# Kernel tuning notes

Hardware: AMD Instinct MI355X
Metric: run time of the kernel (lower is better)

The kernel has to match this reference:

```python
import jax, jax.numpy as jnp
import numpy as np

BLOCK = 16          # NVFP4 block size along contraction dim
FP4_MAX = 6.0       # max magnitude of E2M1
FP8_MAX = 448.0     # max magnitude of float8_e4m3fn

_LEVELS = jnp.array([0.0, 0.5, 1.0, 1.5, 2.0, 3.0, 4.0, 6.0], dtype=jnp.float32)
_MIDS   = jnp.array([0.25, 0.75, 1.25, 1.75, 2.5, 3.5, 5.0], dtype=jnp.float32)


def quantize_dequant_nvfp4(t, global_scale):
    """Fake-quantize t (last dim % 16 == 0) to NVFP4: per-16-block fp8-e4m3
    scale times global fp32 scale, values snapped to the E2M1 grid."""
    shp = t.shape
    tb = t.reshape(shp[:-1] + (shp[-1] // BLOCK, BLOCK))
    amax = jnp.max(jnp.abs(tb), axis=-1, keepdims=True)
    # per-block scale, quantized to float8_e4m3fn as in TensorCoreNVFP4Layout
    bs = amax / (FP4_MAX * global_scale)
    bs8 = bs.astype(jnp.float8_e4m3fn).astype(jnp.float32)
    scale = bs8 * global_scale                       # effective dequant scale
    v = tb / jnp.maximum(scale, 1e-12)
    sign = jnp.sign(v)
    a = jnp.clip(jnp.abs(v), 0.0, FP4_MAX)
    idx = jnp.sum(a[..., None] > _MIDS, axis=-1)     # nearest E2M1 level
    q = _LEVELS[idx] * sign * scale
    return q.reshape(shp)


def setup_inputs() -> dict:
    key = jax.random.key(0)
    kx, kw, kb = jax.random.split(key, 3)
    x = jax.random.normal(kx, (8192, 4096), dtype=jnp.float32)
    weight = jax.random.normal(kw, (4096, 4096), dtype=jnp.float32) * 0.02
    bias = jax.random.normal(kb, (4096,), dtype=jnp.float32) * 0.02
    # global scales (weight_scale_2 / input_scale): amax / (6 * 448)
    input_scale = jnp.max(jnp.abs(x)) / (FP4_MAX * FP8_MAX)
    weight_scale = jnp.max(jnp.abs(weight)) / (FP4_MAX * FP8_MAX)
    return {"x": x, "weight": weight, "bias": bias,
            "input_scale": input_scale, "weight_scale": weight_scale}


def reference(x, weight, bias, input_scale, weight_scale):
    xq = quantize_dequant_nvfp4(x, input_scale)      # [T, K]
    wq = quantize_dequant_nvfp4(weight, weight_scale)  # [N, K]
    return jnp.einsum('tk,nk->tn', xq, wq) + bias    # F.linear
```

## Files before the change

### kernel.cpp

```cpp
#include <hip/hip_runtime.h>
#include <hip/hip_bf16.h>
#include <stdint.h>

typedef __attribute__((ext_vector_type(8))) __bf16 bf16x8;
typedef __attribute__((ext_vector_type(4))) float f32x4;

#define BM 256
#define BN 256
#define BKT 32
#define SLOT 16384


__device__ __forceinline__ float fp8_e4m3_rne(float x) {
  if (x < 0.015625f) {
    return rintf(x * 512.0f) * 0.001953125f;
  }
  uint32_t u = __float_as_uint(x);
  uint32_t keep = u & 0xFFF00000u;
  uint32_t rem  = u & 0x000FFFFFu;
  uint32_t lsb  = (u >> 20) & 1u;
  if (rem > 0x80000u || (rem == 0x80000u && lsb)) keep += 0x100000u;
  return __uint_as_float(keep);
}

__device__ __forceinline__ float snap_lvl(float a) {
  if (a > 5.0f)  return 6.0f;
  if (a > 3.5f)  return 4.0f;
  if (a > 2.5f)  return 3.0f;
  if (a > 1.75f) return 2.0f;
  if (a > 1.25f) return 1.5f;
  if (a > 0.75f) return 1.0f;
  if (a > 0.25f) return 0.5f;
  return 0.0f;
}

__global__ __launch_bounds__(256) void quant_nvfp4(
    const float* __restrict__ in, unsigned short* __restrict__ out,
    const float* __restrict__ gsp, int nblk) {
  int b = blockIdx.x * 256 + threadIdx.x;
  if (b >= nblk) return;
  float gs = gsp[0];
  const float4* p = reinterpret_cast<const float4*>(in) + (size_t)b * 4;
  float v[16];
#pragma unroll
  for (int i = 0; i < 4; ++i) {
    float4 t4 = p[i];
    v[i * 4 + 0] = t4.x; v[i * 4 + 1] = t4.y;
    v[i * 4 + 2] = t4.z; v[i * 4 + 3] = t4.w;
  }
  float amax = 0.0f;
#pragma unroll
  for (int i = 0; i < 16; ++i) amax = fmaxf(amax, fabsf(v[i]));
  float bs8 = fp8_e4m3_rne(amax / (6.0f * gs));
  float scale = fmaxf(bs8 * gs, 1e-12f);
  unsigned short o[16];
#pragma unroll
  for (int i = 0; i < 16; ++i) {
    float q = v[i] / scale;
    float a = fminf(fabsf(q), 6.0f);
    float val = copysignf(snap_lvl(a) * bs8, q);
    o[i] = (unsigned short)(__float_as_uint(val) >> 16);
  }
  uint4 w0 = make_uint4((uint32_t)o[0] | ((uint32_t)o[1] << 16),
                        (uint32_t)o[2] | ((uint32_t)o[3] << 16),
                        (uint32_t)o[4] | ((uint32_t)o[5] << 16),
                        (uint32_t)o[6] | ((uint32_t)o[7] << 16));
  uint4 w1 = make_uint4((uint32_t)o[8]  | ((uint32_t)o[9]  << 16),
                        (uint32_t)o[10] | ((uint32_t)o[11] << 16),
                        (uint32_t)o[12] | ((uint32_t)o[13] << 16),
                        (uint32_t)o[14] | ((uint32_t)o[15] << 16));
  uint4* op = reinterpret_cast<uint4*>(out + (size_t)b * 16);
  op[0] = w0;
  op[1] = w1;
}


__device__ __forceinline__ void async_lds16(const void* g, void* l) {
  __builtin_amdgcn_global_load_lds((__attribute__((address_space(1))) void*)(g),
                                   (__attribute__((address_space(3))) void*)(l),
                                   16, 0, 0);
}

#define SB asm volatile("" ::: "memory")
#define VMC(S) asm volatile("s_waitcnt vmcnt(" S ")" ::: "memory")

#define STAGE_TILE(s, so) {                                                    \
    char* _la = (char*)As + (so);                                              \
    char* _lb = (char*)Bs + (so);                                              \
    async_lds16(pA0 + (size_t)(s) * BKT, _la + lo0);                           \
    async_lds16(pB0 + (size_t)(s) * BKT, _lb + lo0);                           \
    async_lds16(pA1 + (size_t)(s) * BKT, _la + lo1);                           \
    async_lds16(pB1 + (size_t)(s) * BKT, _lb + lo1);                           \
  }

#define CTILE(SOFF) do {                                                       \
    bf16x8 bfr[4], afr[8];                                                     \
    _Pragma("unroll") for (int ni = 0; ni < 4; ++ni)                           \
      bfr[ni] = *(const bf16x8*)((const char*)Bs + offB[ni] + (SOFF));         \
    _Pragma("unroll") for (int mi = 0; mi < 8; ++mi)                           \
      afr[mi] = *(const bf16x8*)((const char*)As + offA[mi] + (SOFF));         \
    _Pragma("unroll") for (int mi = 0; mi < 8; ++mi)                           \
      _Pragma("unroll") for (int ni = 0; ni < 4; ++ni)                         \
        acc[mi][ni] = __builtin_amdgcn_mfma_f32_16x16x32_bf16(                 \
            afr[mi], bfr[ni], acc[mi][ni], 0, 0, 0);                           \
  } while (0)

__global__ __launch_bounds__(512, 2) void gemm_bt_bf16(
    const unsigned short* __restrict__ A, const unsigned short* __restrict__ B,
    const float* __restrict__ bias, const float* __restrict__ gsx,
    const float* __restrict__ gsw, float* __restrict__ C,
    int M, int N, int K) {
  __shared__ __align__(16) unsigned short As[5 * 8192];
  __shared__ __align__(16) unsigned short Bs[5 * 8192];

  const int t = threadIdx.x;
  const int l = t & 63;
  const int w = t >> 6;
  const int wm = w >> 2, wn = w & 3;

  const int nbn = N / BN;
  const int nwg = (M / BM) * nbn;
  const int cpx = nwg >> 3;
  int bid = blockIdx.x;
  int logical = (bid & 7) * cpx + (bid >> 3);
  const int bm = logical / nbn, bn = logical % nbn;
  const int brow = bm * BM, bcol = bn * BN;

  unsigned int b0 = (unsigned int)t * 16u;
  unsigned int b1 = b0 + 8192u;
  unsigned int bp0 = b0 ^ (((b0 >> 7) & 3u) << 4);
  unsigned int bp1 = b1 ^ (((b1 >> 7) & 3u) << 4);
  const unsigned int lo0 = b0, lo1 = b1;
  const unsigned short* pA0 = A + (size_t)(brow + (bp0 >> 6)) * K + ((bp0 & 63u) >> 1);
  const unsigned short* pA1 = A + (size_t)(brow + (bp1 >> 6)) * K + ((bp1 & 63u) >> 1);
  const unsigned short* pB0 = B + (size_t)(bcol + (bp0 >> 6)) * K + ((bp0 & 63u) >> 1);
  const unsigned short* pB1 = B + (size_t)(bcol + (bp1 >> 6)) * K + ((bp1 & 63u) >> 1);

  unsigned int offA[8], offB[4];
#pragma unroll
  for (int mi = 0; mi < 8; ++mi) {
    unsigned int r = wm * 128 + mi * 16 + (l & 15);
    unsigned int q = r * 64 + ((l >> 4) << 4);
    offA[mi] = q ^ (((q >> 7) & 3u) << 4);
  }
#pragma unroll
  for (int ni = 0; ni < 4; ++ni) {
    unsigned int r = wn * 64 + ni * 16 + (l & 15);
    unsigned int q = r * 64 + ((l >> 4) << 4);
    offB[ni] = q ^ (((q >> 7) & 3u) << 4);
  }

  f32x4 acc[8][4] = {};

  STAGE_TILE(0, 0);
  STAGE_TILE(1, SLOT);
  STAGE_TILE(2, 2 * SLOT);

  int sa = 0;
#pragma unroll 1
  for (int w2 = 0; w2 < 62; ++w2) {
    int T = 2 * w2;
    int sb = sa + 1; if (sb >= 5) sb -= 5;
    int s3 = sa + 3; if (s3 >= 5) s3 -= 5;
    int s4 = sa + 4; if (s4 >= 5) s4 -= 5;
    SB; VMC("4"); __builtin_amdgcn_s_barrier(); SB;
    STAGE_TILE(T + 3, s3 * SLOT);
    CTILE(sa * SLOT);
    STAGE_TILE(T + 4, s4 * SLOT);
    CTILE(sb * SLOT);
    sa += 2; if (sa >= 5) sa -= 5;
  }
  SB; VMC("4"); __builtin_amdgcn_s_barrier(); SB;
  STAGE_TILE(127, 2 * SLOT);
  CTILE(4 * SLOT);
  CTILE(0 * SLOT);
  SB; VMC("0"); __builtin_amdgcn_s_barrier(); SB;
  CTILE(1 * SLOT);
  CTILE(2 * SLOT);

  const float gscale = gsx[0] * gsw[0];
  float bias_r[4];
#pragma unroll
  for (int ni = 0; ni < 4; ++ni)
    bias_r[ni] = bias[bcol + wn * 64 + ni * 16 + (l & 15)];
#pragma unroll
  for (int mi = 0; mi < 8; ++mi) {
#pragma unroll
    for (int ni = 0; ni < 4; ++ni) {
#pragma unroll
      for (int r = 0; r < 4; ++r) {
        int row = brow + wm * 128 + mi * 16 + (l >> 4) * 4 + r;
        int col = bcol + wn * 64 + ni * 16 + (l & 15);
        C[(size_t)row * N + col] = acc[mi][ni][r] * gscale + bias_r[ni];
      }
    }
  }
}


extern "C" void kernel_launch(void* const* d_in, const int* in_sizes, int n_in,
                              void* d_out, int out_size, void* d_ws, size_t ws_size,
                              hipStream_t stream) {
  const float* x    = (const float*)d_in[0];
  const float* wgt  = (const float*)d_in[1];
  const float* bias = (const float*)d_in[2];
  const float* isc  = (const float*)d_in[3];
  const float* wsc  = (const float*)d_in[4];
  float* out = (float*)d_out;

  const int N = in_sizes[2];
  const int K = in_sizes[1] / N;
  const int M = in_sizes[0] / K;

  unsigned short* Aq = (unsigned short*)d_ws;
  unsigned short* Bq = Aq + (size_t)M * K;

  int nblkA = M * K / 16;
  quant_nvfp4<<<(nblkA + 255) / 256, 256, 0, stream>>>(x, Aq, isc, nblkA);
  int nblkB = N * K / 16;
  quant_nvfp4<<<(nblkB + 255) / 256, 256, 0, stream>>>(wgt, Bq, wsc, nblkB);

  dim3 grid((M / BM) * (N / BN));
  gemm_bt_bf16<<<grid, 512, 0, stream>>>(Aq, Bq, bias, isc, wsc, out, M, N, K);
}
```

Measured before the change: 337.2 us.

## Pack quantized weights in MFMA fragment order and load B directly to registers

The weight quantizer now writes B in a pre-packed layout that matches the MFMA fragment order. This lets the GEMM load B fragments straight from global memory into registers with double-buffered register sets, skipping the LDS staging for B. The A operand keeps LDS staging but moves to a 3-slot ring, and uses inline ds_read with fine-grained lgkmcnt waits, sched barriers and setprio so MFMAs can interleave with LDS reads. This frees LDS and cuts LDS traffic, but B global loads are now issued per wave, so latency hiding depends on the one-tile-ahead register prefetch.

```diff
diff --git a/kernel.cpp b/kernel.cpp
--- a/kernel.cpp
+++ b/kernel.cpp
@@ -4,6 +4,7 @@
 
 typedef __attribute__((ext_vector_type(8))) __bf16 bf16x8;
 typedef __attribute__((ext_vector_type(4))) float f32x4;
+typedef __attribute__((ext_vector_type(4))) unsigned int u32x4;
 
 #define BM 256
 #define BN 256
@@ -34,33 +35,36 @@
   return 0.0f;
 }
 
+__device__ __forceinline__ void quant16(const float* __restrict__ src, float gs,
+                                        unsigned short* o) {
+  float v[16];
+#pragma unroll
+  for (int i = 0; i < 4; ++i) {
+    float4 t4 = reinterpret_cast<const float4*>(src)[i];
+    v[i * 4 + 0] = t4.x; v[i * 4 + 1] = t4.y;
+    v[i * 4 + 2] = t4.z; v[i * 4 + 3] = t4.w;
+  }
+  float amax = 0.0f;
+#pragma unroll
+  for (int i = 0; i < 16; ++i) amax = fmaxf(amax, fabsf(v[i]));
+  float bs8 = fp8_e4m3_rne(amax / (6.0f * gs));
+  float scale = fmaxf(bs8 * gs, 1e-12f);
+#pragma unroll
+  for (int i = 0; i < 16; ++i) {
+    float q = v[i] / scale;
+    float a = fminf(fabsf(q), 6.0f);
+    float val = copysignf(snap_lvl(a) * bs8, q);
+    o[i] = (unsigned short)(__float_as_uint(val) >> 16);
+  }
+}
+
 __global__ __launch_bounds__(256) void quant_nvfp4(
     const float* __restrict__ in, unsigned short* __restrict__ out,
     const float* __restrict__ gsp, int nblk) {
   int b = blockIdx.x * 256 + threadIdx.x;
   if (b >= nblk) return;
-  float gs = gsp[0];
-  const float4* p = reinterpret_cast<const float4*>(in) + (size_t)b * 4;
-  float v[16];
-#pragma unroll
-  for (int i = 0; i < 4; ++i) {
-    float4 t4 = p[i];
-    v[i * 4 + 0] = t4.x; v[i * 4 + 1] = t4.y;
-    v[i * 4 + 2] = t4.z; v[i * 4 + 3] = t4.w;
-  }
-  float amax = 0.0f;
-#pragma unroll
-  for (int i = 0; i < 16; ++i) amax = fmaxf(amax, fabsf(v[i]));
-  float bs8 = fp8_e4m3_rne(amax / (6.0f * gs));
-  float scale = fmaxf(bs8 * gs, 1e-12f);
   unsigned short o[16];
-#pragma unroll
-  for (int i = 0; i < 16; ++i) {
-    float q = v[i] / scale;
-    float a = fminf(fabsf(q), 6.0f);
-    float val = copysignf(snap_lvl(a) * bs8, q);
-    o[i] = (unsigned short)(__float_as_uint(val) >> 16);
-  }
+  quant16(in + (size_t)b * 16, gsp[0], o);
   uint4 w0 = make_uint4((uint32_t)o[0] | ((uint32_t)o[1] << 16),
                         (uint32_t)o[2] | ((uint32_t)o[3] << 16),
                         (uint32_t)o[4] | ((uint32_t)o[5] << 16),
@@ -74,6 +78,33 @@
   op[1] = w1;
 }
 
+__global__ __launch_bounds__(256) void quant_packB(
+    const float* __restrict__ in, unsigned short* __restrict__ out,
+    const float* __restrict__ gsp, int K, int nblk) {
+  int t = blockIdx.x * 256 + threadIdx.x;
+  if (t >= nblk) return;
+  const int K16 = K >> 4;
+  int nr   = t & 15;
+  int rest = t >> 4;
+  int kb   = rest % K16;
+  int n16  = rest / K16;
+  int row  = n16 * 16 + nr;
+  unsigned short o[16];
+  quant16(in + (size_t)row * K + (size_t)kb * 16, gsp[0], o);
+  const int KT = K >> 5;
+  size_t u0 = ((size_t)(n16 * KT + (kb >> 1)) * 64 + (kb & 1) * 32 + nr) * 8;
+  uint4 w0 = make_uint4((uint32_t)o[0] | ((uint32_t)o[1] << 16),
+                        (uint32_t)o[2] | ((uint32_t)o[3] << 16),
+                        (uint32_t)o[4] | ((uint32_t)o[5] << 16),
+                        (uint32_t)o[6] | ((uint32_t)o[7] << 16));
+  uint4 w1 = make_uint4((uint32_t)o[8]  | ((uint32_t)o[9]  << 16),
+                        (uint32_t)o[10] | ((uint32_t)o[11] << 16),
+                        (uint32_t)o[12] | ((uint32_t)o[13] << 16),
+                        (uint32_t)o[14] | ((uint32_t)o[15] << 16));
+  *reinterpret_cast<uint4*>(out + u0)       = w0;
+  *reinterpret_cast<uint4*>(out + u0 + 128) = w1;
+}
+
 
 __device__ __forceinline__ void async_lds16(const void* g, void* l) {
   __builtin_amdgcn_global_load_lds((__attribute__((address_space(1))) void*)(g),
@@ -81,42 +112,68 @@
                                    16, 0, 0);
 }
 
-#define SB asm volatile("" ::: "memory")
+#define DSR(dst, a) asm volatile("ds_read_b128 %0, %1" : "=v"(dst) : "v"(a))
+#define LGKM(N) do { asm volatile("s_waitcnt lgkmcnt(" #N ")" ::: "memory"); \
+                     __builtin_amdgcn_sched_barrier(0); } while (0)
 #define VMC(S) asm volatile("s_waitcnt vmcnt(" S ")" ::: "memory")
-
-#define STAGE_TILE(s, so) {                                                    \
-    char* _la = (char*)As + (so);                                              \
-    char* _lb = (char*)Bs + (so);                                              \
-    async_lds16(pA0 + (size_t)(s) * BKT, _la + lo0);                           \
-    async_lds16(pB0 + (size_t)(s) * BKT, _lb + lo0);                           \
-    async_lds16(pA1 + (size_t)(s) * BKT, _la + lo1);                           \
-    async_lds16(pB1 + (size_t)(s) * BKT, _lb + lo1);                           \
-  }
-
-#define CTILE(SOFF) do {                                                       \
-    bf16x8 bfr[4], afr[8];                                                     \
-    _Pragma("unroll") for (int ni = 0; ni < 4; ++ni)                           \
-      bfr[ni] = *(const bf16x8*)((const char*)Bs + offB[ni] + (SOFF));         \
-    _Pragma("unroll") for (int mi = 0; mi < 8; ++mi)                           \
-      afr[mi] = *(const bf16x8*)((const char*)As + offA[mi] + (SOFF));         \
-    _Pragma("unroll") for (int mi = 0; mi < 8; ++mi)                           \
-      _Pragma("unroll") for (int ni = 0; ni < 4; ++ni)                         \
-        acc[mi][ni] = __builtin_amdgcn_mfma_f32_16x16x32_bf16(                 \
-            afr[mi], bfr[ni], acc[mi][ni], 0, 0, 0);                           \
+#define SCB __builtin_amdgcn_sched_barrier(0)
+#define BCB(x) __builtin_bit_cast(bf16x8, x)
+
+#define BLOAD(dst, ni, Tn) \
+  asm volatile("global_load_dwordx4 %0, %1, off" \
+               : "=v"(dst) : "v"(bAddr[ni] + (uint64_t)(Tn) * 1024))
+
+#define MF4(mi, ar, Bc0, Bc1, Bc2, Bc3) do {                                   \
+    acc[mi][0] = __builtin_amdgcn_mfma_f32_16x16x32_bf16(BCB(ar), BCB(Bc0), acc[mi][0], 0, 0, 0); \
+    acc[mi][1] = __builtin_amdgcn_mfma_f32_16x16x32_bf16(BCB(ar), BCB(Bc1), acc[mi][1], 0, 0, 0); \
+    acc[mi][2] = __builtin_amdgcn_mfma_f32_16x16x32_bf16(BCB(ar), BCB(Bc2), acc[mi][2], 0, 0, 0); \
+    acc[mi][3] = __builtin_amdgcn_mfma_f32_16x16x32_bf16(BCB(ar), BCB(Bc3), acc[mi][3], 0, 0, 0); \
   } while (0)
 
+#define GTILE(T, C0, C1, C2, C3, N0, N1, N2, N3, DOB, DOA, VMS) do {           \
+    VMC(VMS); SCB;                                                             \
+    __builtin_amdgcn_s_barrier(); SCB;                                         \
+    if (DOB) { BLOAD(N0, 0, (T) + 1); BLOAD(N1, 1, (T) + 1);                   \
+               BLOAD(N2, 2, (T) + 1); BLOAD(N3, 3, (T) + 1); }                 \
+    SCB;                                                                       \
+    if (DOA) {                                                                 \
+      char* _la = (char*)As + (((T) + 2) % 3) * SLOT;                          \
+      async_lds16(pA0 + (size_t)((T) + 2) * BKT, _la + lo0);                   \
+      async_lds16(pA1 + (size_t)((T) + 2) * BKT, _la + lo1);                   \
+    }                                                                          \
+    SCB;                                                                       \
+    {                                                                          \
+      const unsigned soff = (unsigned)(((T) % 3) * SLOT);                      \
+      u32x4 a0, a1, a2, a3, a4, a5, a6, a7;                                    \
+      DSR(a0, adA[0] + soff); DSR(a1, adA[1] + soff);                          \
+      DSR(a2, adA[2] + soff); DSR(a3, adA[3] + soff);                          \
+      DSR(a4, adA[4] + soff); DSR(a5, adA[5] + soff);                          \
+      DSR(a6, adA[6] + soff); DSR(a7, adA[7] + soff);                          \
+      SCB;                                                                     \
+      LGKM(7); __builtin_amdgcn_s_setprio(1); MF4(0, a0, C0, C1, C2, C3);      \
+      LGKM(6); MF4(1, a1, C0, C1, C2, C3);                                     \
+      LGKM(5); MF4(2, a2, C0, C1, C2, C3);                                     \
+      LGKM(4); MF4(3, a3, C0, C1, C2, C3);                                     \
+      LGKM(3); MF4(4, a4, C0, C1, C2, C3);                                     \
+      LGKM(2); MF4(5, a5, C0, C1, C2, C3);                                     \
+      LGKM(1); MF4(6, a6, C0, C1, C2, C3);                                     \
+      LGKM(0); MF4(7, a7, C0, C1, C2, C3);                                     \
+      __builtin_amdgcn_s_setprio(0); SCB;                                      \
+    }                                                                          \
+  } while (0)
+
 __global__ __launch_bounds__(512, 2) void gemm_bt_bf16(
-    const unsigned short* __restrict__ A, const unsigned short* __restrict__ B,
+    const unsigned short* __restrict__ A, const unsigned short* __restrict__ PB,
     const float* __restrict__ bias, const float* __restrict__ gsx,
     const float* __restrict__ gsw, float* __restrict__ C,
     int M, int N, int K) {
-  __shared__ __align__(16) unsigned short As[5 * 8192];
-  __shared__ __align__(16) unsigned short Bs[5 * 8192];
+  __shared__ __align__(16) unsigned short As[3 * 8192];
 
   const int t = threadIdx.x;
   const int l = t & 63;
   const int w = t >> 6;
   const int wm = w >> 2, wn = w & 3;
+  const int KT = K >> 5;
 
   const int nbn = N / BN;
   const int nwg = (M / BM) * nbn;
@@ -133,50 +190,44 @@
   const unsigned int lo0 = b0, lo1 = b1;
   const unsigned short* pA0 = A + (size_t)(brow + (bp0 >> 6)) * K + ((bp0 & 63u) >> 1);
   const unsigned short* pA1 = A + (size_t)(brow + (bp1 >> 6)) * K + ((bp1 & 63u) >> 1);
-  const unsigned short* pB0 = B + (size_t)(bcol + (bp0 >> 6)) * K + ((bp0 & 63u) >> 1);
-  const unsigned short* pB1 = B + (size_t)(bcol + (bp1 >> 6)) * K + ((bp1 & 63u) >> 1);
-
-  unsigned int offA[8], offB[4];
+
+  const unsigned baseAu = (unsigned)(uintptr_t)(&As[0]);
+  unsigned int adA[8];
 #pragma unroll
   for (int mi = 0; mi < 8; ++mi) {
     unsigned int r = wm * 128 + mi * 16 + (l & 15);
     unsigned int q = r * 64 + ((l >> 4) << 4);
-    offA[mi] = q ^ (((q >> 7) & 3u) << 4);
-  }
+    adA[mi] = baseAu + (q ^ (((q >> 7) & 3u) << 4));
+  }
+
+  uint64_t bAddr[4];
 #pragma unroll
   for (int ni = 0; ni < 4; ++ni) {
-    unsigned int r = wn * 64 + ni * 16 + (l & 15);
-    unsigned int q = r * 64 + ((l >> 4) << 4);
-    offB[ni] = q ^ (((q >> 7) & 3u) << 4);
+    int n16 = (bcol >> 4) + wn * 4 + ni;
+    bAddr[ni] = (uint64_t)(uintptr_t)PB + (((uint64_t)n16 * KT) * 64 + (uint64_t)l) * 16;
   }
 
   f32x4 acc[8][4] = {};
-
-  STAGE_TILE(0, 0);
-  STAGE_TILE(1, SLOT);
-  STAGE_TILE(2, 2 * SLOT);
-
-  int sa = 0;
+  u32x4 bP0, bP1, bP2, bP3;
+  u32x4 bQ0, bQ1, bQ2, bQ3;
+
+  async_lds16(pA0, (char*)As + lo0);
+  async_lds16(pA1, (char*)As + lo1);
+  SCB;
+  BLOAD(bP0, 0, 0); BLOAD(bP1, 1, 0); BLOAD(bP2, 2, 0); BLOAD(bP3, 3, 0);
+  SCB;
+  async_lds16(pA0 + BKT, (char*)As + SLOT + lo0);
+  async_lds16(pA1 + BKT, (char*)As + SLOT + lo1);
+  SCB;
+
 #pragma unroll 1
-  for (int w2 = 0; w2 < 62; ++w2) {
-    int T = 2 * w2;
-    int sb = sa + 1; if (sb >= 5) sb -= 5;
-    int s3 = sa + 3; if (s3 >= 5) s3 -= 5;
-    int s4 = sa + 4; if (s4 >= 5) s4 -= 5;
-    SB; VMC("4"); __builtin_amdgcn_s_barrier(); SB;
-    STAGE_TILE(T + 3, s3 * SLOT);
-    CTILE(sa * SLOT);
-    STAGE_TILE(T + 4, s4 * SLOT);
-    CTILE(sb * SLOT);
-    sa += 2; if (sa >= 5) sa -= 5;
-  }
-  SB; VMC("4"); __builtin_amdgcn_s_barrier(); SB;
-  STAGE_TILE(127, 2 * SLOT);
-  CTILE(4 * SLOT);
-  CTILE(0 * SLOT);
-  SB; VMC("0"); __builtin_amdgcn_s_barrier(); SB;
-  CTILE(1 * SLOT);
-  CTILE(2 * SLOT);
+  for (int i = 0; i < 63; ++i) {
+    const int T = 2 * i;
+    GTILE(T,     bP0, bP1, bP2, bP3, bQ0, bQ1, bQ2, bQ3, 1, 1, "2");
+    GTILE(T + 1, bQ0, bQ1, bQ2, bQ3, bP0, bP1, bP2, bP3, 1, 1, "2");
+  }
+  GTILE(126, bP0, bP1, bP2, bP3, bQ0, bQ1, bQ2, bQ3, 1, 0, "2");
+  GTILE(127, bQ0, bQ1, bQ2, bQ3, bP0, bP1, bP2, bP3, 0, 0, "0");
 
   const float gscale = gsx[0] * gsw[0];
   float bias_r[4];
@@ -218,7 +269,7 @@
   int nblkA = M * K / 16;
   quant_nvfp4<<<(nblkA + 255) / 256, 256, 0, stream>>>(x, Aq, isc, nblkA);
   int nblkB = N * K / 16;
-  quant_nvfp4<<<(nblkB + 255) / 256, 256, 0, stream>>>(wgt, Bq, wsc, nblkB);
+  quant_packB<<<(nblkB + 255) / 256, 256, 0, stream>>>(wgt, Bq, wsc, K, nblkB);
 
   dim3 grid((M / BM) * (N / BN));
   gemm_bt_bf16<<<grid, 512, 0, stream>>>(Aq, Bq, bias, isc, wsc, out, M, N, K);
```

Measured after the change: 281.7 us. 16.5% less time.
